# Performance work log

Hardware: AMD Instinct MI355X
Metric: run time of the kernel (lower is better)

The kernel has to match this reference:

```python
import jax, jax.numpy as jnp
import numpy as np

ALPHA = 0.5
BETA = 0.5
N_NODES = 100000
N_EDGES = 1600000
D = 64  # out_channels


def setup_inputs() -> dict:
    key = jax.random.key(0)
    ks = jax.random.split(key, 8)
    z_in = jax.random.normal(ks[0], (N_NODES, D + 1), dtype=jnp.float32)
    z_out = jax.random.normal(ks[1], (N_NODES, D + 1), dtype=jnp.float32)
    z_self = jax.random.normal(ks[2], (N_NODES, D), dtype=jnp.float32)
    edge_index = jax.random.randint(ks[3], (2, N_EDGES), 0, N_NODES, dtype=jnp.int64)
    s = 1.0 / np.sqrt(D)  # torch Linear default init scale
    W_in = jax.random.uniform(ks[4], (D, D), jnp.float32, -s, s)
    b_in = jax.random.uniform(ks[5], (D,), jnp.float32, -s, s)
    W_out = jax.random.uniform(ks[6], (D, D), jnp.float32, -s, s)
    b_out = jax.random.uniform(ks[7], (D,), jnp.float32, -s, s)
    return {"z_in": z_in, "z_out": z_out, "z_self": z_self,
            "W_in": W_in, "b_in": b_in, "W_out": W_out, "b_out": b_out,
            "edge_index": edge_index}


def _norm_degree(deg, n_unique):
    # degree / (num_unique_nodes - 1), then L2-normalize over dim 0 (F.normalize)
    d = deg / (n_unique - 1.0)
    nrm = jnp.maximum(jnp.linalg.norm(d), 1e-12)
    return d / nrm


def reference(z_in, z_out, z_self, W_in, b_in, W_out, b_out, edge_index):
    src = edge_index[0]
    dst = edge_index[1]
    n = z_self.shape[0]
    ones = jnp.ones(src.shape, jnp.float32)
    deg_out = jax.ops.segment_sum(ones, src, num_segments=n)  # out-degree per node
    deg_in = jax.ops.segment_sum(ones, dst, num_segments=n)   # in-degree per node
    present = jnp.zeros((n,), bool).at[edge_index.reshape(-1)].set(True)
    n_unique = present.sum().astype(jnp.float32)  # len(set(edge_index.flatten()))
    real_degreeout = _norm_degree(deg_out, n_unique)[src]  # [E]
    real_degreein = _norm_degree(deg_in, n_unique)[dst]    # [E]
    # small aligned linears on gathered node features
    align_out_dst = z_self[dst] @ W_out.T + b_out  # [E, D]
    align_in_src = z_self[src] @ W_in.T + b_in     # [E, D]
    value = ((real_degreeout + z_out[src, -1]) * BETA
             + jnp.sum(z_out[src, :-1] * align_out_dst, axis=1) * ALPHA
             + (real_degreein + z_in[dst, -1]) * BETA
             + jnp.sum(align_in_src * z_in[dst, :-1], axis=1) * ALPHA)
    return jax.nn.sigmoid(value)
```

## Files before the change

kernel.cpp:

```cpp
#include <hip/hip_runtime.h>
#include <hip/hip_fp16.h>
#include <math.h>

#define ALPHA_C 0.5f
#define BETA_C  0.5f
#define NPART   256
#define NQUART  4

typedef _Float16 half8 __attribute__((ext_vector_type(8)));
typedef _Float16 half2v __attribute__((ext_vector_type(2)));
typedef float f32x4 __attribute__((ext_vector_type(4)));

__device__ __forceinline__ int swz(int row, int byteoff) {
    return byteoff ^ ((row & 7) << 4);
}

__global__ __launch_bounds__(256) void k_hist(
        const int* __restrict__ eidx, unsigned int* __restrict__ scr,
        int N, int E, int Q, int Wd, int chunk) {
    const int s = blockIdx.x;
    const int role = blockIdx.y;
    const int dir = role & 1;
    const int q = role >> 1;
    extern __shared__ unsigned int lds[];
    for (int w = threadIdx.x; w < Wd; w += blockDim.x) lds[w] = 0;
    __syncthreads();
    const int base = q * Q;
    const int hi = min(N - base, Q);
    const int* __restrict__ arr = eidx + (size_t)dir * E;
    const int start = s * chunk;
    const int end = min(E, start + chunk);
    const int4* __restrict__ a4 = (const int4*)arr;
    const int v1 = end >> 2;
    for (int v = (start >> 2) + threadIdx.x; v < v1; v += blockDim.x) {
        int4 x = a4[v];
        int l;
        l = x.x - base; if ((unsigned)l < (unsigned)hi) atomicAdd(&lds[l >> 1], 1u << ((l & 1) * 16));
        l = x.y - base; if ((unsigned)l < (unsigned)hi) atomicAdd(&lds[l >> 1], 1u << ((l & 1) * 16));
        l = x.z - base; if ((unsigned)l < (unsigned)hi) atomicAdd(&lds[l >> 1], 1u << ((l & 1) * 16));
        l = x.w - base; if ((unsigned)l < (unsigned)hi) atomicAdd(&lds[l >> 1], 1u << ((l & 1) * 16));
    }
    for (int i = (v1 << 2) + threadIdx.x; i < end; i += blockDim.x) {
        int l = arr[i] - base;
        if ((unsigned)l < (unsigned)hi) atomicAdd(&lds[l >> 1], 1u << ((l & 1) * 16));
    }
    __syncthreads();
    unsigned int* __restrict__ dst = scr + ((size_t)role * gridDim.x + s) * Wd;
    for (int w = threadIdx.x; w < Wd; w += blockDim.x) dst[w] = lds[w];
}

__global__ __launch_bounds__(256) void k_fold(
        const unsigned int* __restrict__ scr,
        float* __restrict__ deg_out, float* __restrict__ deg_in,
        float* __restrict__ partials, int N, int Q, int Wd, int S) {
    float so = 0.f, si = 0.f;
    for (int n = blockIdx.x * blockDim.x + threadIdx.x; n < N;
         n += gridDim.x * blockDim.x) {
        const int q = n / Q, l = n - q * Q;
        const int w = l >> 1, sh = (l & 1) * 16;
        const unsigned int* __restrict__ p0 = scr + ((size_t)(q * 2 + 0) * S) * Wd + w;
        const unsigned int* __restrict__ p1 = scr + ((size_t)(q * 2 + 1) * S) * Wd + w;
        unsigned int a = 0, b = 0;
        for (int s = 0; s < S; ++s) {
            a += (p0[(size_t)s * Wd] >> sh) & 0xFFFFu;
            b += (p1[(size_t)s * Wd] >> sh) & 0xFFFFu;
        }
        float fa = (float)a, fb = (float)b;
        deg_out[n] = fa;
        deg_in[n] = fb;
        so = fmaf(fa, fa, so);
        si = fmaf(fb, fb, si);
    }
#pragma unroll
    for (int off = 32; off; off >>= 1) {
        so += __shfl_xor(so, off);
        si += __shfl_xor(si, off);
    }
    __shared__ float sm[2][4];
    int lane = threadIdx.x & 63, w = threadIdx.x >> 6;
    if (lane == 0) { sm[0][w] = so; sm[1][w] = si; }
    __syncthreads();
    if (threadIdx.x == 0) {
        partials[blockIdx.x]         = sm[0][0] + sm[0][1] + sm[0][2] + sm[0][3];
        partials[NPART + blockIdx.x] = sm[1][0] + sm[1][1] + sm[1][2] + sm[1][3];
    }
}

__global__ __launch_bounds__(256) void k_finish(
        const float* __restrict__ partials, float* __restrict__ inv_nrm) {
    int t = threadIdx.x;
    float so = partials[t], si = partials[NPART + t];
#pragma unroll
    for (int off = 32; off; off >>= 1) {
        so += __shfl_xor(so, off);
        si += __shfl_xor(si, off);
    }
    __shared__ float sm[2][4];
    int lane = t & 63, w = t >> 6;
    if (lane == 0) { sm[0][w] = so; sm[1][w] = si; }
    __syncthreads();
    if (t == 0) {
        float a = sm[0][0] + sm[0][1] + sm[0][2] + sm[0][3];
        float b = sm[1][0] + sm[1][1] + sm[1][2] + sm[1][3];
        inv_nrm[0] = (a > 0.f) ? rsqrtf(a) : 0.f;
        inv_nrm[1] = (b > 0.f) ? rsqrtf(b) : 0.f;
    }
}

__global__ __launch_bounds__(256) void k_nodes(
        const float* __restrict__ z_in, const float* __restrict__ z_out,
        const float* __restrict__ z_self,
        const float* __restrict__ W_in, const float* __restrict__ b_in,
        const float* __restrict__ W_out, const float* __restrict__ b_out,
        const float* __restrict__ deg_out, const float* __restrict__ deg_in,
        const float* __restrict__ inv_nrm,
        _Float16* __restrict__ P_src, _Float16* __restrict__ P_dst,
        float* __restrict__ s_src, float* __restrict__ s_dst, int N) {
    __shared__ _Float16 smem[16384];
    char* lzo = (char*)smem;
    char* lzi = (char*)smem + 8192;
    char* lwo = (char*)smem + 16384;
    char* lwi = (char*)smem + 24576;
    char* lps = (char*)smem;
    char* lpd = (char*)smem + 16384;

    const int tid = threadIdx.x;
    const int lane = tid & 63;
    const int wid = tid >> 6;
    const int r = lane & 15, g = lane >> 4;
    const int base = blockIdx.x * 64;
    const int wrow = wid * 16;

#pragma unroll
    for (int it = 0; it < 8; ++it) {
        int flat = it * 256 + tid;
        int row = flat >> 5;
        int c2 = (flat & 31) * 2;
        int grow = min(base + row, N - 1);
        const float* zr = z_out + (size_t)grow * 65;
        half2v ho = { (_Float16)zr[c2], (_Float16)zr[c2 + 1] };
        *(half2v*)(lzo + row * 128 + swz(row, c2 * 2)) = ho;
        const float* zr2 = z_in + (size_t)grow * 65;
        half2v hi = { (_Float16)zr2[c2], (_Float16)zr2[c2 + 1] };
        *(half2v*)(lzi + row * 128 + swz(row, c2 * 2)) = hi;
    }
#pragma unroll
    for (int it = 0; it < 16; ++it) {
        int flat = it * 256 + tid;
        int k = flat >> 6, n = flat & 63;
        *(_Float16*)(lwo + n * 128 + swz(n, k * 2)) = (_Float16)W_out[k * 64 + n];
        *(_Float16*)(lwi + n * 128 + swz(n, k * 2)) = (_Float16)W_in [k * 64 + n];
    }
    half8 bO[2], bI[2];
#pragma unroll
    for (int s = 0; s < 2; ++s)
#pragma unroll
        for (int j = 0; j < 8; ++j) {
            int k = 32 * s + 8 * g + j;
            bO[s][j] = (r == 0) ? (_Float16)b_out[k] : (_Float16)0.f;
            bI[s][j] = (r == 0) ? (_Float16)b_in [k] : (_Float16)0.f;
        }
    __syncthreads();

    half8 AO[2], AI[2];
#pragma unroll
    for (int s = 0; s < 2; ++s) {
        int arow = wrow + r;
        int off = arow * 128 + swz(arow, s * 64 + g * 16);
        AO[s] = *(half8*)(lzo + off);
        AI[s] = *(half8*)(lzi + off);
    }
    f32x4 aO[4], aI[4], abO = (f32x4)0.f, abI = (f32x4)0.f;
#pragma unroll
    for (int t = 0; t < 4; ++t) { aO[t] = (f32x4)0.f; aI[t] = (f32x4)0.f; }
#pragma unroll
    for (int s = 0; s < 2; ++s) {
#pragma unroll
        for (int t = 0; t < 4; ++t) {
            int n = 16 * t + r;
            int off = n * 128 + swz(n, s * 64 + g * 16);
            half8 BO = *(half8*)(lwo + off);
            aO[t] = __builtin_amdgcn_mfma_f32_16x16x32_f16(AO[s], BO, aO[t], 0, 0, 0);
            half8 BI = *(half8*)(lwi + off);
            aI[t] = __builtin_amdgcn_mfma_f32_16x16x32_f16(AI[s], BI, aI[t], 0, 0, 0);
        }
        abO = __builtin_amdgcn_mfma_f32_16x16x32_f16(AO[s], bO[s], abO, 0, 0, 0);
        abI = __builtin_amdgcn_mfma_f32_16x16x32_f16(AI[s], bI[s], abI, 0, 0, 0);
    }
    __syncthreads();

#pragma unroll
    for (int t = 0; t < 4; ++t)
#pragma unroll
        for (int rr = 0; rr < 4; ++rr) {
            int lrow = wrow + 4 * g + rr;
            int col2 = (16 * t + r) * 2;
            *(_Float16*)(lps + lrow * 256 + swz(lrow, col2)) = (_Float16)aO[t][rr];
            *(_Float16*)(lpd + lrow * 256 + swz(lrow, 128 + col2)) = (_Float16)aI[t][rr];
        }
#pragma unroll
    for (int it = 0; it < 8; ++it) {
        int flat = it * 256 + tid;
        int row = flat >> 5;
        int c2 = (flat & 31) * 2;
        int grow = min(base + row, N - 1);
        float2 v = *(const float2*)(z_self + (size_t)grow * 64 + c2);
        half2v h = { (_Float16)v.x, (_Float16)v.y };
        *(half2v*)(lps + row * 256 + swz(row, 128 + c2 * 2)) = h;
        *(half2v*)(lpd + row * 256 + swz(row, c2 * 2)) = h;
    }
    if (r == 0) {
        const float i0 = inv_nrm[0], i1 = inv_nrm[1];
#pragma unroll
        for (int rr = 0; rr < 4; ++rr) {
            int m = base + wrow + 4 * g + rr;
            if (m < N) {
                s_src[m] = BETA_C * fmaf(deg_out[m], i0, z_out[(size_t)m * 65 + 64])
                         + ALPHA_C * abO[rr];
                s_dst[m] = BETA_C * fmaf(deg_in[m],  i1, z_in [(size_t)m * 65 + 64])
                         + ALPHA_C * abI[rr];
            }
        }
    }
    __syncthreads();

#pragma unroll
    for (int it = 0; it < 4; ++it) {
        int lrow = it * 16 + (tid >> 4);
        int seg = tid & 15;
        int m = base + lrow;
        if (m < N) {
            half8 v = *(half8*)(lps + lrow * 256 + swz(lrow, seg * 16));
            *(half8*)(P_src + (size_t)m * 128 + seg * 8) = v;
            half8 v2 = *(half8*)(lpd + lrow * 256 + swz(lrow, seg * 16));
            *(half8*)(P_dst + (size_t)m * 128 + seg * 8) = v2;
        }
    }
}

__global__ __launch_bounds__(256) void k_edges(
        const int* __restrict__ eidx,
        const _Float16* __restrict__ P_src, const _Float16* __restrict__ P_dst,
        const float* __restrict__ s_src, const float* __restrict__ s_dst,
        float* __restrict__ out, int E) {
    const int sub = threadIdx.x & 15;
    const int e = blockIdx.x * (blockDim.x >> 4) + (threadIdx.x >> 4);
    if (e >= E) return;
    const int s = eidx[e];
    const int d = eidx[E + e];
    const half8 a = *(const half8*)(P_src + (size_t)s * 128 + sub * 8);
    const half8 b = *(const half8*)(P_dst + (size_t)d * 128 + sub * 8);
    float acc = 0.f;
#pragma unroll
    for (int j = 0; j < 8; ++j)
        acc = fmaf((float)a[j], (float)b[j], acc);
    acc += __shfl_xor(acc, 8);
    acc += __shfl_xor(acc, 4);
    acc += __shfl_xor(acc, 2);
    acc += __shfl_xor(acc, 1);
    if (sub == 0) {
        float v = fmaf(ALPHA_C, acc, s_src[s] + s_dst[d]);
        out[e] = 1.0f / (1.0f + __expf(-v));
    }
}

extern "C" void kernel_launch(void* const* d_in, const int* in_sizes, int n_in,
                              void* d_out, int out_size, void* d_ws, size_t ws_size,
                              hipStream_t stream) {
    const float* z_in   = (const float*)d_in[0];
    const float* z_out  = (const float*)d_in[1];
    const float* z_self = (const float*)d_in[2];
    const float* W_in   = (const float*)d_in[3];
    const float* b_in   = (const float*)d_in[4];
    const float* W_out  = (const float*)d_in[5];
    const float* b_out  = (const float*)d_in[6];
    const int*   eidx   = (const int*)d_in[7];

    const int N = in_sizes[2] / 64;
    const int E = in_sizes[7] / 2;

    const int Q = (N + NQUART - 1) / NQUART;
    const int Wd = (Q + 1) / 2;
    int S = (E + 49999) / 50000;
    if (S < 1) S = 1;
    int chunk = ((E + S - 1) / S + 3) & ~3;

    float* ws       = (float*)d_ws;
    float* deg_out  = ws;
    float* deg_in   = ws + (size_t)N;
    float* s_src    = ws + 2 * (size_t)N;
    float* s_dst    = ws + 3 * (size_t)N;
    _Float16* P_src = (_Float16*)(ws + 4 * (size_t)N);
    _Float16* P_dst = P_src + (size_t)N * 128;
    float* partials = (float*)(P_dst + (size_t)N * 128);
    float* inv_nrm  = partials + 2 * NPART;
    unsigned int* scr = (unsigned int*)P_src;

    dim3 hgrid(S, 2 * NQUART);
    k_hist<<<hgrid, 256, (size_t)Wd * 4, stream>>>(eidx, scr, N, E, Q, Wd, chunk);
    k_fold<<<NPART, 256, 0, stream>>>(scr, deg_out, deg_in, partials, N, Q, Wd, S);
    k_finish<<<1, 256, 0, stream>>>(partials, inv_nrm);
    k_nodes<<<(N + 63) / 64, 256, 0, stream>>>(z_in, z_out, z_self, W_in, b_in,
                                               W_out, b_out, deg_out, deg_in,
                                               inv_nrm, P_src, P_dst,
                                               s_src, s_dst, N);
    k_edges<<<(E + 15) / 16, 256, 0, stream>>>(eidx, P_src, P_dst,
                                               s_src, s_dst, (float*)d_out, E);
}
```

Before: 205.8 us.

## Pre-convert weights once, process two edges per group with fdot2

A new one-block kernel converts and transposes W_in and W_out to fp16 once in workspace. k_nodes then reads the MFMA B operands directly from global memory or cache instead of staging them through swizzled LDS in every block. The edge kernel now handles two edges per 16-lane group, with vectorized index loads, packed fp16 dot products via fdot2, and interleaved reductions, to raise memory-level parallelism on the random gathers. This costs an extra launch and gives up LDS reuse of the weights.

```diff
diff --git a/kernel.cpp b/kernel.cpp
--- a/kernel.cpp
+++ b/kernel.cpp
@@ -13,6 +13,16 @@
 
 __device__ __forceinline__ int swz(int row, int byteoff) {
     return byteoff ^ ((row & 7) << 4);
+}
+
+__global__ __launch_bounds__(256) void k_prep(
+        const float* __restrict__ W_in, const float* __restrict__ W_out,
+        _Float16* __restrict__ w16i, _Float16* __restrict__ w16o) {
+    for (int i = threadIdx.x; i < 4096; i += 256) {
+        int k = i >> 6, n = i & 63;
+        w16o[n * 64 + k] = (_Float16)W_out[k * 64 + n];
+        w16i[n * 64 + k] = (_Float16)W_in [k * 64 + n];
+    }
 }
 
 __global__ __launch_bounds__(256) void k_hist(
@@ -110,8 +120,8 @@
 __global__ __launch_bounds__(256) void k_nodes(
         const float* __restrict__ z_in, const float* __restrict__ z_out,
         const float* __restrict__ z_self,
-        const float* __restrict__ W_in, const float* __restrict__ b_in,
-        const float* __restrict__ W_out, const float* __restrict__ b_out,
+        const _Float16* __restrict__ w16i, const _Float16* __restrict__ w16o,
+        const float* __restrict__ b_in, const float* __restrict__ b_out,
         const float* __restrict__ deg_out, const float* __restrict__ deg_in,
         const float* __restrict__ inv_nrm,
         _Float16* __restrict__ P_src, _Float16* __restrict__ P_dst,
@@ -119,8 +129,6 @@
     __shared__ _Float16 smem[16384];
     char* lzo = (char*)smem;
     char* lzi = (char*)smem + 8192;
-    char* lwo = (char*)smem + 16384;
-    char* lwi = (char*)smem + 24576;
     char* lps = (char*)smem;
     char* lpd = (char*)smem + 16384;
 
@@ -144,13 +152,6 @@
         half2v hi = { (_Float16)zr2[c2], (_Float16)zr2[c2 + 1] };
         *(half2v*)(lzi + row * 128 + swz(row, c2 * 2)) = hi;
     }
-#pragma unroll
-    for (int it = 0; it < 16; ++it) {
-        int flat = it * 256 + tid;
-        int k = flat >> 6, n = flat & 63;
-        *(_Float16*)(lwo + n * 128 + swz(n, k * 2)) = (_Float16)W_out[k * 64 + n];
-        *(_Float16*)(lwi + n * 128 + swz(n, k * 2)) = (_Float16)W_in [k * 64 + n];
-    }
     half8 bO[2], bI[2];
 #pragma unroll
     for (int s = 0; s < 2; ++s)
@@ -177,11 +178,10 @@
     for (int s = 0; s < 2; ++s) {
 #pragma unroll
         for (int t = 0; t < 4; ++t) {
-            int n = 16 * t + r;
-            int off = n * 128 + swz(n, s * 64 + g * 16);
-            half8 BO = *(half8*)(lwo + off);
+            int woff = (16 * t + r) * 64 + 32 * s + 8 * g;
+            half8 BO = *(const half8*)(w16o + woff);
             aO[t] = __builtin_amdgcn_mfma_f32_16x16x32_f16(AO[s], BO, aO[t], 0, 0, 0);
-            half8 BI = *(half8*)(lwi + off);
+            half8 BI = *(const half8*)(w16i + woff);
             aI[t] = __builtin_amdgcn_mfma_f32_16x16x32_f16(AI[s], BI, aI[t], 0, 0, 0);
         }
         abO = __builtin_amdgcn_mfma_f32_16x16x32_f16(AO[s], bO[s], abO, 0, 0, 0);
@@ -244,23 +244,41 @@
         const float* __restrict__ s_src, const float* __restrict__ s_dst,
         float* __restrict__ out, int E) {
     const int sub = threadIdx.x & 15;
-    const int e = blockIdx.x * (blockDim.x >> 4) + (threadIdx.x >> 4);
-    if (e >= E) return;
-    const int s = eidx[e];
-    const int d = eidx[E + e];
-    const half8 a = *(const half8*)(P_src + (size_t)s * 128 + sub * 8);
-    const half8 b = *(const half8*)(P_dst + (size_t)d * 128 + sub * 8);
-    float acc = 0.f;
-#pragma unroll
-    for (int j = 0; j < 8; ++j)
-        acc = fmaf((float)a[j], (float)b[j], acc);
-    acc += __shfl_xor(acc, 8);
-    acc += __shfl_xor(acc, 4);
-    acc += __shfl_xor(acc, 2);
-    acc += __shfl_xor(acc, 1);
-    if (sub == 0) {
-        float v = fmaf(ALPHA_C, acc, s_src[s] + s_dst[d]);
-        out[e] = 1.0f / (1.0f + __expf(-v));
+    const int grp = blockIdx.x * (blockDim.x >> 4) + (threadIdx.x >> 4);
+    const int e0 = grp << 1;
+    if (e0 >= E) return;
+    const bool has1 = (e0 + 1) < E;
+    int2 ss = *(const int2*)(eidx + e0);
+    int2 dd = *(const int2*)(eidx + E + e0);
+    const int s1 = has1 ? ss.y : ss.x, d1 = has1 ? dd.y : dd.x;
+    const uint4 a0 = *(const uint4*)(P_src + (size_t)ss.x * 128 + sub * 8);
+    const uint4 b0 = *(const uint4*)(P_dst + (size_t)dd.x * 128 + sub * 8);
+    const uint4 a1 = *(const uint4*)(P_src + (size_t)s1 * 128 + sub * 8);
+    const uint4 b1 = *(const uint4*)(P_dst + (size_t)d1 * 128 + sub * 8);
+    float ssum = 0.f;
+    if (sub < 2) {
+        int s = sub ? s1 : ss.x;
+        int d = sub ? d1 : dd.x;
+        ssum = s_src[s] + s_dst[d];
+    }
+    float acc0 = 0.f, acc1 = 0.f;
+    acc0 = __builtin_amdgcn_fdot2(__builtin_bit_cast(half2v, a0.x), __builtin_bit_cast(half2v, b0.x), acc0, false);
+    acc0 = __builtin_amdgcn_fdot2(__builtin_bit_cast(half2v, a0.y), __builtin_bit_cast(half2v, b0.y), acc0, false);
+    acc0 = __builtin_amdgcn_fdot2(__builtin_bit_cast(half2v, a0.z), __builtin_bit_cast(half2v, b0.z), acc0, false);
+    acc0 = __builtin_amdgcn_fdot2(__builtin_bit_cast(half2v, a0.w), __builtin_bit_cast(half2v, b0.w), acc0, false);
+    acc1 = __builtin_amdgcn_fdot2(__builtin_bit_cast(half2v, a1.x), __builtin_bit_cast(half2v, b1.x), acc1, false);
+    acc1 = __builtin_amdgcn_fdot2(__builtin_bit_cast(half2v, a1.y), __builtin_bit_cast(half2v, b1.y), acc1, false);
+    acc1 = __builtin_amdgcn_fdot2(__builtin_bit_cast(half2v, a1.z), __builtin_bit_cast(half2v, b1.z), acc1, false);
+    acc1 = __builtin_amdgcn_fdot2(__builtin_bit_cast(half2v, a1.w), __builtin_bit_cast(half2v, b1.w), acc1, false);
+#pragma unroll
+    for (int off = 8; off; off >>= 1) {
+        acc0 += __shfl_xor(acc0, off);
+        acc1 += __shfl_xor(acc1, off);
+    }
+    if (sub < 2 && (sub == 0 || has1)) {
+        float acc = sub ? acc1 : acc0;
+        float v = fmaf(ALPHA_C, acc, ssum);
+        out[e0 + sub] = 1.0f / (1.0f + __expf(-v));
     }
 }
 
@@ -294,16 +312,23 @@
     _Float16* P_dst = P_src + (size_t)N * 128;
     float* partials = (float*)(P_dst + (size_t)N * 128);
     float* inv_nrm  = partials + 2 * NPART;
+    _Float16* w16o  = (_Float16*)(partials + 2 * NPART + 16);
+    _Float16* w16i  = w16o + 4096;
     unsigned int* scr = (unsigned int*)P_src;
 
+    k_prep<<<1, 256, 0, stream>>>(W_in, W_out, w16i, w16o);
     dim3 hgrid(S, 2 * NQUART);
     k_hist<<<hgrid, 256, (size_t)Wd * 4, stream>>>(eidx, scr, N, E, Q, Wd, chunk);
     k_fold<<<NPART, 256, 0, stream>>>(scr, deg_out, deg_in, partials, N, Q, Wd, S);
     k_finish<<<1, 256, 0, stream>>>(partials, inv_nrm);
-    k_nodes<<<(N + 63) / 64, 256, 0, stream>>>(z_in, z_out, z_self, W_in, b_in,
-                                               W_out, b_out, deg_out, deg_in,
+    k_nodes<<<(N + 63) / 64, 256, 0, stream>>>(z_in, z_out, z_self, w16i, w16o,
+                                               b_in, b_out, deg_out, deg_in,
                                                inv_nrm, P_src, P_dst,
                                                s_src, s_dst, N);
-    k_edges<<<(E + 15) / 16, 256, 0, stream>>>(eidx, P_src, P_dst,
-                                               s_src, s_dst, (float*)d_out, E);
-}
+    {
+        int groups = (E + 1) / 2;
+        int blocks = (groups + 15) / 16;
+        k_edges<<<blocks, 256, 0, stream>>>(eidx, P_src, P_dst,
+                                            s_src, s_dst, (float*)d_out, E);
+    }
+}
```

Result: slower. 212.9 us (+3.4%).
